# Optimization experiments

Hardware: AMD Instinct MI355X
Metric: run time of the kernel (lower is better)

## Reference

```python
import math
import jax, jax.numpy as jnp
import numpy as np


def bernstein_basis(s, k):
    # s: [N] in [0,1]; returns [N, k] with B_i(s) = C(k-1,i) s^i (1-s)^(k-1-i)
    l = k - 1
    i = jnp.arange(k, dtype=s.dtype)
    comb = jnp.asarray([math.comb(l, ii) for ii in range(k)], dtype=s.dtype)
    return comb * s[:, None] ** i * (1.0 - s[:, None]) ** (l - i)


def setup_inputs() -> dict:
    key = jax.random.key(0)
    k1, k2 = jax.random.split(key)
    N, kx, ky, kz = 1000000, 6, 6, 6
    vertices = jax.random.uniform(k1, (N, 3), dtype=jnp.float32) * 2.0 - 1.0  # in [-1,1]
    p = jax.random.uniform(k2, (3, kx, ky, kz), dtype=jnp.float32)
    return {"vertices": vertices, "p": p}


def reference(vertices, p):
    # vertices: [N,3] in [-1,1]; p: [3,kx,ky,kz]
    kx, ky, kz = p.shape[1], p.shape[2], p.shape[3]
    tar = (vertices + 1.0) * 0.5  # normalize_zero_to_one, [N,3]
    Bx = bernstein_basis(tar[:, 0], kx)  # [N,kx]
    By = bernstein_basis(tar[:, 1], ky)  # [N,ky]
    Bz = bernstein_basis(tar[:, 2], kz)  # [N,kz]
    # staged contraction replacing the kx*ky*kz loop of elementwise kernels
    t1 = jnp.einsum('nk,cijk->ncij', Bz, p)   # [N,3,kx,ky]
    t2 = jnp.einsum('nj,ncij->nci', By, t1)   # [N,3,kx]
    q = jnp.einsum('ni,nci->nc', Bx, t2)      # [N,3]
    q = 2.0 * q - 1.0  # normalize_minus_one_to_one
    return q[None, :, :]  # [1,N,3], matching q.permute(0,2,1)
```

## Files before the change

kernel.cpp:

```cpp
#include <hip/hip_runtime.h>

__device__ __constant__ float Mb[6][6] = {
    { 0.03125f, -0.15625f,  0.3125f, -0.3125f,  0.15625f, -0.03125f},
    { 0.15625f, -0.46875f,  0.3125f,  0.3125f, -0.46875f,  0.15625f},
    { 0.3125f,  -0.3125f,  -0.625f,   0.625f,   0.3125f,  -0.3125f },
    { 0.3125f,   0.3125f,  -0.625f,  -0.625f,   0.3125f,   0.3125f },
    { 0.15625f,  0.46875f,  0.3125f, -0.3125f, -0.46875f, -0.15625f},
    { 0.03125f,  0.15625f,  0.3125f,  0.3125f,  0.15625f,  0.03125f},
};

__global__ __launch_bounds__(256) void ffd_fused(const float* __restrict__ verts,
                                                 const float* __restrict__ p,
                                                 float* __restrict__ out, int N)
{
    __shared__ __align__(16) float b0[648];
    __shared__ __align__(16) float b1[648];
    const int t = threadIdx.x;

    for (int m = t; m < 648; m += 256) b0[m] = p[m];
    __syncthreads();

    for (int m = t; m < 648; m += 256) {
        const int dk = m % 6;
        const int base = (m / 6) * 6;
        float s = 0.f;
        #pragma unroll
        for (int k = 0; k < 6; ++k) s = fmaf(b0[base + k], Mb[k][dk], s);
        b1[m] = s;
    }
    __syncthreads();

    for (int m = t; m < 648; m += 256) {
        const int dk = m % 6;
        const int dj = (m / 6) % 6;
        const int ci = m / 36;
        float s = 0.f;
        #pragma unroll
        for (int j = 0; j < 6; ++j) s = fmaf(b1[(ci * 6 + j) * 6 + dk], Mb[j][dj], s);
        b0[m] = s;
    }
    __syncthreads();

    for (int m = t; m < 648; m += 256) {
        const int dk = m % 6;
        const int dj = (m / 6) % 6;
        const int di = (m / 36) % 6;
        const int c  = m / 216;
        float s = 0.f;
        #pragma unroll
        for (int i = 0; i < 6; ++i) s = fmaf(b0[((c * 6 + i) * 6 + dj) * 6 + dk], Mb[i][di], s);
        s *= 2.0f;
        if (di == 0 && dj == 0 && dk == 0) s -= 1.0f;
        b1[m] = s;
    }
    __syncthreads();

    const long long v0 = ((long long)blockIdx.x * 256 + t) * 4;
    if (v0 >= N) return;

    float x[4], y[4], z[4];
    const bool full = (v0 + 4 <= N);
    if (full) {
        const float4* vp = (const float4*)(verts + v0 * 3);
        const float4 f0 = vp[0], f1 = vp[1], f2 = vp[2];
        x[0] = f0.x; y[0] = f0.y; z[0] = f0.z;
        x[1] = f0.w; y[1] = f1.x; z[1] = f1.y;
        x[2] = f1.z; y[2] = f1.w; z[2] = f2.x;
        x[3] = f2.y; y[3] = f2.z; z[3] = f2.w;
    } else {
        for (int v = 0; v < 4; ++v) {
            long long n = v0 + v; if (n >= N) n = N - 1;
            x[v] = verts[n * 3 + 0]; y[v] = verts[n * 3 + 1]; z[v] = verts[n * 3 + 2];
        }
    }

    float res[12];
    #pragma unroll 1
    for (int c = 0; c < 3; ++c) {
        float q[4];
        #pragma unroll 1
        for (int ii = 0; ii < 6; ++ii) {
            const int i = 5 - ii;
            const float4* blk = (const float4*)(b1 + (c * 6 + i) * 36);
            float a[36];
            #pragma unroll
            for (int r = 0; r < 9; ++r) {
                const float4 f = blk[r];
                a[r * 4 + 0] = f.x; a[r * 4 + 1] = f.y;
                a[r * 4 + 2] = f.z; a[r * 4 + 3] = f.w;
            }
            float tj[4];
            #pragma unroll
            for (int jj = 0; jj < 6; ++jj) {
                const int j = 5 - jj;
                const float* Ak = a + j * 6;
                #pragma unroll
                for (int v = 0; v < 4; ++v) {
                    float s = fmaf(Ak[5], z[v], Ak[4]);
                    s = fmaf(s, z[v], Ak[3]);
                    s = fmaf(s, z[v], Ak[2]);
                    s = fmaf(s, z[v], Ak[1]);
                    s = fmaf(s, z[v], Ak[0]);
                    tj[v] = (jj == 0) ? s : fmaf(tj[v], y[v], s);
                }
            }
            #pragma unroll
            for (int v = 0; v < 4; ++v)
                q[v] = (ii == 0) ? tj[v] : fmaf(q[v], x[v], tj[v]);
        }
        #pragma unroll
        for (int v = 0; v < 4; ++v) res[v * 3 + c] = q[v];
    }

    if (full) {
        float4* op = (float4*)(out + v0 * 3);
        op[0] = make_float4(res[0], res[1], res[2],  res[3]);
        op[1] = make_float4(res[4], res[5], res[6],  res[7]);
        op[2] = make_float4(res[8], res[9], res[10], res[11]);
    } else {
        for (int v = 0; v < 4; ++v) {
            const long long n = v0 + v;
            if (n < N) {
                out[n * 3 + 0] = res[v * 3 + 0];
                out[n * 3 + 1] = res[v * 3 + 1];
                out[n * 3 + 2] = res[v * 3 + 2];
            }
        }
    }
}

extern "C" void kernel_launch(void* const* d_in, const int* in_sizes, int n_in,
                              void* d_out, int out_size, void* d_ws, size_t ws_size,
                              hipStream_t stream)
{
    const float* verts = (const float*)d_in[0];
    const float* p     = (const float*)d_in[1];
    float* out = (float*)d_out;
    const int N = in_sizes[0] / 3;

    const int nthreads = (N + 3) / 4;
    const int blocks = (nthreads + 255) / 256;
    ffd_fused<<<blocks, 256, 0, stream>>>(verts, p, out, N);
}
```

Baseline: 78.87 us.

## Split coefficient precompute into separate kernel and read coefficients via scalar loads

Moves the per-block Bernstein-to-monomial coefficient transform into a single-block kernel that writes 648 coefficients to workspace. The eval kernel then reads them with wave-uniform offsets (readfirstlane) so they can be fetched as scalar loads instead of from LDS. It also drops from 4 to 2 vertices per thread and unrolls the channel loop. This removes redundant per-block transform work and syncs, at the cost of an extra launch and half the per-thread work.

```diff
diff --git a/kernel.cpp b/kernel.cpp
--- a/kernel.cpp
+++ b/kernel.cpp
@@ -9,12 +9,11 @@
     { 0.03125f,  0.15625f,  0.3125f,  0.3125f,  0.15625f,  0.03125f},
 };
 
-__global__ __launch_bounds__(256) void ffd_fused(const float* __restrict__ verts,
-                                                 const float* __restrict__ p,
-                                                 float* __restrict__ out, int N)
+__global__ __launch_bounds__(256) void ffd_coeffs(const float* __restrict__ p,
+                                                  float* __restrict__ A)
 {
-    __shared__ __align__(16) float b0[648];
-    __shared__ __align__(16) float b1[648];
+    __shared__ float b0[648];
+    __shared__ float b1[648];
     const int t = threadIdx.x;
 
     for (int m = t; m < 648; m += 256) b0[m] = p[m];
@@ -51,74 +50,76 @@
         for (int i = 0; i < 6; ++i) s = fmaf(b0[((c * 6 + i) * 6 + dj) * 6 + dk], Mb[i][di], s);
         s *= 2.0f;
         if (di == 0 && dj == 0 && dk == 0) s -= 1.0f;
-        b1[m] = s;
+        A[m] = s;
     }
-    __syncthreads();
+}
 
-    const long long v0 = ((long long)blockIdx.x * 256 + t) * 4;
+__global__ __launch_bounds__(256) void ffd_eval(const float* __restrict__ verts,
+                                                const float* __restrict__ A,
+                                                float* __restrict__ out, int N)
+{
+    const long long v0 = ((long long)blockIdx.x * 256 + threadIdx.x) * 2;
     if (v0 >= N) return;
 
-    float x[4], y[4], z[4];
-    const bool full = (v0 + 4 <= N);
+    float x[2], y[2], z[2];
+    const bool full = (v0 + 2 <= N);
     if (full) {
-        const float4* vp = (const float4*)(verts + v0 * 3);
-        const float4 f0 = vp[0], f1 = vp[1], f2 = vp[2];
-        x[0] = f0.x; y[0] = f0.y; z[0] = f0.z;
-        x[1] = f0.w; y[1] = f1.x; z[1] = f1.y;
-        x[2] = f1.z; y[2] = f1.w; z[2] = f2.x;
-        x[3] = f2.y; y[3] = f2.z; z[3] = f2.w;
+        const float2* vp = (const float2*)(verts + v0 * 3);
+        const float2 f0 = vp[0], f1 = vp[1], f2 = vp[2];
+        x[0] = f0.x; y[0] = f0.y; z[0] = f1.x;
+        x[1] = f1.y; y[1] = f2.x; z[1] = f2.y;
     } else {
-        for (int v = 0; v < 4; ++v) {
+        for (int v = 0; v < 2; ++v) {
             long long n = v0 + v; if (n >= N) n = N - 1;
             x[v] = verts[n * 3 + 0]; y[v] = verts[n * 3 + 1]; z[v] = verts[n * 3 + 2];
         }
     }
 
-    float res[12];
-    #pragma unroll 1
+    float res[6];
+    #pragma unroll
     for (int c = 0; c < 3; ++c) {
-        float q[4];
+        float q0 = 0.f, q1 = 0.f;
         #pragma unroll 1
         for (int ii = 0; ii < 6; ++ii) {
             const int i = 5 - ii;
-            const float4* blk = (const float4*)(b1 + (c * 6 + i) * 36);
+            const int off = __builtin_amdgcn_readfirstlane((c * 6 + i) * 36);
+            const float* __restrict__ Ab = A + off;
             float a[36];
             #pragma unroll
-            for (int r = 0; r < 9; ++r) {
-                const float4 f = blk[r];
-                a[r * 4 + 0] = f.x; a[r * 4 + 1] = f.y;
-                a[r * 4 + 2] = f.z; a[r * 4 + 3] = f.w;
-            }
-            float tj[4];
+            for (int r = 0; r < 36; ++r) a[r] = Ab[r];
+
+            float t0 = 0.f, t1 = 0.f;
             #pragma unroll
             for (int jj = 0; jj < 6; ++jj) {
                 const int j = 5 - jj;
                 const float* Ak = a + j * 6;
-                #pragma unroll
-                for (int v = 0; v < 4; ++v) {
-                    float s = fmaf(Ak[5], z[v], Ak[4]);
-                    s = fmaf(s, z[v], Ak[3]);
-                    s = fmaf(s, z[v], Ak[2]);
-                    s = fmaf(s, z[v], Ak[1]);
-                    s = fmaf(s, z[v], Ak[0]);
-                    tj[v] = (jj == 0) ? s : fmaf(tj[v], y[v], s);
-                }
+                float s0 = fmaf(Ak[5], z[0], Ak[4]);
+                s0 = fmaf(s0, z[0], Ak[3]);
+                s0 = fmaf(s0, z[0], Ak[2]);
+                s0 = fmaf(s0, z[0], Ak[1]);
+                s0 = fmaf(s0, z[0], Ak[0]);
+                float s1 = fmaf(Ak[5], z[1], Ak[4]);
+                s1 = fmaf(s1, z[1], Ak[3]);
+                s1 = fmaf(s1, z[1], Ak[2]);
+                s1 = fmaf(s1, z[1], Ak[1]);
+                s1 = fmaf(s1, z[1], Ak[0]);
+                t0 = (jj == 0) ? s0 : fmaf(t0, y[0], s0);
+                t1 = (jj == 0) ? s1 : fmaf(t1, y[1], s1);
             }
-            #pragma unroll
-            for (int v = 0; v < 4; ++v)
-                q[v] = (ii == 0) ? tj[v] : fmaf(q[v], x[v], tj[v]);
+            q0 = (ii == 0) ? t0 : fmaf(q0, x[0], t0);
+            q1 = (ii == 0) ? t1 : fmaf(q1, x[1], t1);
         }
-        #pragma unroll
-        for (int v = 0; v < 4; ++v) res[v * 3 + c] = q[v];
+        res[c]     = q0;
+        res[3 + c] = q1;
     }
 
     if (full) {
-        float4* op = (float4*)(out + v0 * 3);
-        op[0] = make_float4(res[0], res[1], res[2],  res[3]);
-        op[1] = make_float4(res[4], res[5], res[6],  res[7]);
-        op[2] = make_float4(res[8], res[9], res[10], res[11]);
+        float2* op = (float2*)(out + v0 * 3);
+        op[0] = make_float2(res[0], res[1]);
+        op[1] = make_float2(res[2], res[3]);
+        op[2] = make_float2(res[4], res[5]);
     } else {
-        for (int v = 0; v < 4; ++v) {
+        for (int v = 0; v < 2; ++v) {
             const long long n = v0 + v;
             if (n < N) {
                 out[n * 3 + 0] = res[v * 3 + 0];
@@ -136,9 +137,12 @@
     const float* verts = (const float*)d_in[0];
     const float* p     = (const float*)d_in[1];
     float* out = (float*)d_out;
+    float* A   = (float*)d_ws;
     const int N = in_sizes[0] / 3;
 
-    const int nthreads = (N + 3) / 4;
+    ffd_coeffs<<<1, 256, 0, stream>>>(p, A);
+
+    const int nthreads = (N + 1) / 2;
     const int blocks = (nthreads + 255) / 256;
-    ffd_fused<<<blocks, 256, 0, stream>>>(verts, p, out, N);
+    ffd_eval<<<blocks, 256, 0, stream>>>(verts, A, out, N);
 }
```

Result: slower. 80.71 us (+2.3%).

## Split coefficient precompute into separate kernel and load coefficients via scalar loads

Applied to the files above, without the earlier changes.

Moves the Bernstein-to-monomial coefficient transform out of every block into a single-block precompute kernel that writes to workspace. The evaluation kernel then reads the 36-coefficient slices with inline-asm scalar loads into SGPRs instead of LDS reads, and fully unrolls the channel and i loops. This removes the redundant per-block shared-memory setup and barriers and the LDS traffic, at the cost of a second launch, a hard wait on each scalar load batch, and higher scalar register pressure.

```diff
diff --git a/kernel.cpp b/kernel.cpp
--- a/kernel.cpp
+++ b/kernel.cpp
@@ -9,12 +9,11 @@
     { 0.03125f,  0.15625f,  0.3125f,  0.3125f,  0.15625f,  0.03125f},
 };
 
-__global__ __launch_bounds__(256) void ffd_fused(const float* __restrict__ verts,
-                                                 const float* __restrict__ p,
-                                                 float* __restrict__ out, int N)
+__global__ __launch_bounds__(256) void ffd_coeffs(const float* __restrict__ p,
+                                                  float* __restrict__ A)
 {
-    __shared__ __align__(16) float b0[648];
-    __shared__ __align__(16) float b1[648];
+    __shared__ float b0[648];
+    __shared__ float b1[648];
     const int t = threadIdx.x;
 
     for (int m = t; m < 648; m += 256) b0[m] = p[m];
@@ -51,10 +50,18 @@
         for (int i = 0; i < 6; ++i) s = fmaf(b0[((c * 6 + i) * 6 + dj) * 6 + dk], Mb[i][di], s);
         s *= 2.0f;
         if (di == 0 && dj == 0 && dk == 0) s -= 1.0f;
-        b1[m] = s;
+        A[m] = s;
     }
-    __syncthreads();
+}
 
+typedef float f16v __attribute__((ext_vector_type(16)));
+typedef float f4v  __attribute__((ext_vector_type(4)));
+
+__global__ __launch_bounds__(256) void ffd_eval(const float* __restrict__ verts,
+                                                const float* __restrict__ A,
+                                                float* __restrict__ out, int N)
+{
+    const int t = threadIdx.x;
     const long long v0 = ((long long)blockIdx.x * 256 + t) * 4;
     if (v0 >= N) return;
 
@@ -75,20 +82,29 @@
     }
 
     float res[12];
-    #pragma unroll 1
+    #pragma unroll
     for (int c = 0; c < 3; ++c) {
         float q[4];
-        #pragma unroll 1
+        #pragma unroll
         for (int ii = 0; ii < 6; ++ii) {
             const int i = 5 - ii;
-            const float4* blk = (const float4*)(b1 + (c * 6 + i) * 36);
+            const float* Ab = A + (c * 6 + i) * 36;
+            f16v a0, a1; f4v a2;
+            asm volatile(
+                "s_load_dwordx16 %0, %3, 0x0\n\t"
+                "s_load_dwordx16 %1, %3, 0x40\n\t"
+                "s_load_dwordx4  %2, %3, 0x80\n\t"
+                "s_waitcnt lgkmcnt(0)"
+                : "=s"(a0), "=s"(a1), "=s"(a2)
+                : "s"(Ab));
             float a[36];
             #pragma unroll
-            for (int r = 0; r < 9; ++r) {
-                const float4 f = blk[r];
-                a[r * 4 + 0] = f.x; a[r * 4 + 1] = f.y;
-                a[r * 4 + 2] = f.z; a[r * 4 + 3] = f.w;
-            }
+            for (int r = 0; r < 16; ++r) a[r] = a0[r];
+            #pragma unroll
+            for (int r = 0; r < 16; ++r) a[16 + r] = a1[r];
+            #pragma unroll
+            for (int r = 0; r < 4; ++r) a[32 + r] = a2[r];
+
             float tj[4];
             #pragma unroll
             for (int jj = 0; jj < 6; ++jj) {
@@ -136,9 +152,12 @@
     const float* verts = (const float*)d_in[0];
     const float* p     = (const float*)d_in[1];
     float* out = (float*)d_out;
+    float* A   = (float*)d_ws;
     const int N = in_sizes[0] / 3;
+
+    ffd_coeffs<<<1, 256, 0, stream>>>(p, A);
 
     const int nthreads = (N + 3) / 4;
     const int blocks = (nthreads + 255) / 256;
-    ffd_fused<<<blocks, 256, 0, stream>>>(verts, p, out, N);
+    ffd_eval<<<blocks, 256, 0, stream>>>(verts, A, out, N);
 }
```

Result: slower. 104.2 us (+32.1%).

## Process eight vertices per thread with double-buffered LDS coefficient loads

Applied to the files above, without the earlier changes.

Each thread now handles eight vertices instead of four, so every coefficient block read from shared memory is reused across twice as many vertices. The i-loop is also split into ping-pong register buffers, so the next 36-float block is loaded while the current one is being evaluated, and the c loop is fully unrolled. The aim is to cut LDS traffic per vertex and hide LDS latency. In exchange, register pressure rises sharply (two 36-float buffers plus 8-wide state), which can lower occupancy, and the block count halves, so the per-block setup of the transformed coefficients is spread over more vertices.

```diff
diff --git a/kernel.cpp b/kernel.cpp
--- a/kernel.cpp
+++ b/kernel.cpp
@@ -55,70 +55,118 @@
     }
     __syncthreads();
 
-    const long long v0 = ((long long)blockIdx.x * 256 + t) * 4;
+    const long long v0 = ((long long)blockIdx.x * 256 + t) * 8;
     if (v0 >= N) return;
 
-    float x[4], y[4], z[4];
-    const bool full = (v0 + 4 <= N);
+    float x[8], y[8], z[8];
+    const bool full = (v0 + 8 <= N);
     if (full) {
         const float4* vp = (const float4*)(verts + v0 * 3);
-        const float4 f0 = vp[0], f1 = vp[1], f2 = vp[2];
+        float4 f0 = vp[0], f1 = vp[1], f2 = vp[2], f3 = vp[3], f4 = vp[4], f5 = vp[5];
         x[0] = f0.x; y[0] = f0.y; z[0] = f0.z;
         x[1] = f0.w; y[1] = f1.x; z[1] = f1.y;
         x[2] = f1.z; y[2] = f1.w; z[2] = f2.x;
         x[3] = f2.y; y[3] = f2.z; z[3] = f2.w;
+        x[4] = f3.x; y[4] = f3.y; z[4] = f3.z;
+        x[5] = f3.w; y[5] = f4.x; z[5] = f4.y;
+        x[6] = f4.z; y[6] = f4.w; z[6] = f5.x;
+        x[7] = f5.y; y[7] = f5.z; z[7] = f5.w;
     } else {
-        for (int v = 0; v < 4; ++v) {
+        for (int v = 0; v < 8; ++v) {
             long long n = v0 + v; if (n >= N) n = N - 1;
             x[v] = verts[n * 3 + 0]; y[v] = verts[n * 3 + 1]; z[v] = verts[n * 3 + 2];
         }
     }
 
-    float res[12];
-    #pragma unroll 1
+    float res[24];
+    #pragma unroll
     for (int c = 0; c < 3; ++c) {
-        float q[4];
-        #pragma unroll 1
-        for (int ii = 0; ii < 6; ++ii) {
-            const int i = 5 - ii;
-            const float4* blk = (const float4*)(b1 + (c * 6 + i) * 36);
-            float a[36];
+        float q[8];
+        #pragma unroll
+        for (int v = 0; v < 8; ++v) q[v] = 0.f;
+
+        float aA[36], aB[36];
+        {
+            const float4* blk = (const float4*)(b1 + c * 216 + 5 * 36);
             #pragma unroll
             for (int r = 0; r < 9; ++r) {
                 const float4 f = blk[r];
-                a[r * 4 + 0] = f.x; a[r * 4 + 1] = f.y;
-                a[r * 4 + 2] = f.z; a[r * 4 + 3] = f.w;
+                aA[r * 4 + 0] = f.x; aA[r * 4 + 1] = f.y;
+                aA[r * 4 + 2] = f.z; aA[r * 4 + 3] = f.w;
             }
-            float tj[4];
-            #pragma unroll
-            for (int jj = 0; jj < 6; ++jj) {
-                const int j = 5 - jj;
-                const float* Ak = a + j * 6;
+        }
+        #pragma unroll 1
+        for (int m = 0; m < 3; ++m) {
+            const int i0 = 5 - 2 * m;
+            {
+                const float4* blk = (const float4*)(b1 + c * 216 + (i0 - 1) * 36);
                 #pragma unroll
-                for (int v = 0; v < 4; ++v) {
-                    float s = fmaf(Ak[5], z[v], Ak[4]);
-                    s = fmaf(s, z[v], Ak[3]);
-                    s = fmaf(s, z[v], Ak[2]);
-                    s = fmaf(s, z[v], Ak[1]);
-                    s = fmaf(s, z[v], Ak[0]);
-                    tj[v] = (jj == 0) ? s : fmaf(tj[v], y[v], s);
+                for (int r = 0; r < 9; ++r) {
+                    const float4 f = blk[r];
+                    aB[r * 4 + 0] = f.x; aB[r * 4 + 1] = f.y;
+                    aB[r * 4 + 2] = f.z; aB[r * 4 + 3] = f.w;
                 }
             }
-            #pragma unroll
-            for (int v = 0; v < 4; ++v)
-                q[v] = (ii == 0) ? tj[v] : fmaf(q[v], x[v], tj[v]);
+            {
+                float tj[8];
+                #pragma unroll
+                for (int jj = 0; jj < 6; ++jj) {
+                    const int j = 5 - jj;
+                    const float* Ak = aA + j * 6;
+                    #pragma unroll
+                    for (int v = 0; v < 8; ++v) {
+                        float s = fmaf(Ak[5], z[v], Ak[4]);
+                        s = fmaf(s, z[v], Ak[3]);
+                        s = fmaf(s, z[v], Ak[2]);
+                        s = fmaf(s, z[v], Ak[1]);
+                        s = fmaf(s, z[v], Ak[0]);
+                        tj[v] = (jj == 0) ? s : fmaf(tj[v], y[v], s);
+                    }
+                }
+                #pragma unroll
+                for (int v = 0; v < 8; ++v) q[v] = fmaf(q[v], x[v], tj[v]);
+            }
+            if (m < 2) {
+                const float4* blk = (const float4*)(b1 + c * 216 + (i0 - 2) * 36);
+                #pragma unroll
+                for (int r = 0; r < 9; ++r) {
+                    const float4 f = blk[r];
+                    aA[r * 4 + 0] = f.x; aA[r * 4 + 1] = f.y;
+                    aA[r * 4 + 2] = f.z; aA[r * 4 + 3] = f.w;
+                }
+            }
+            {
+                float tj[8];
+                #pragma unroll
+                for (int jj = 0; jj < 6; ++jj) {
+                    const int j = 5 - jj;
+                    const float* Ak = aB + j * 6;
+                    #pragma unroll
+                    for (int v = 0; v < 8; ++v) {
+                        float s = fmaf(Ak[5], z[v], Ak[4]);
+                        s = fmaf(s, z[v], Ak[3]);
+                        s = fmaf(s, z[v], Ak[2]);
+                        s = fmaf(s, z[v], Ak[1]);
+                        s = fmaf(s, z[v], Ak[0]);
+                        tj[v] = (jj == 0) ? s : fmaf(tj[v], y[v], s);
+                    }
+                }
+                #pragma unroll
+                for (int v = 0; v < 8; ++v) q[v] = fmaf(q[v], x[v], tj[v]);
+            }
         }
         #pragma unroll
-        for (int v = 0; v < 4; ++v) res[v * 3 + c] = q[v];
+        for (int v = 0; v < 8; ++v) res[v * 3 + c] = q[v];
     }
 
     if (full) {
         float4* op = (float4*)(out + v0 * 3);
-        op[0] = make_float4(res[0], res[1], res[2],  res[3]);
-        op[1] = make_float4(res[4], res[5], res[6],  res[7]);
-        op[2] = make_float4(res[8], res[9], res[10], res[11]);
+        #pragma unroll
+        for (int r = 0; r < 6; ++r)
+            op[r] = make_float4(res[r * 4 + 0], res[r * 4 + 1],
+                                res[r * 4 + 2], res[r * 4 + 3]);
     } else {
-        for (int v = 0; v < 4; ++v) {
+        for (int v = 0; v < 8; ++v) {
             const long long n = v0 + v;
             if (n < N) {
                 out[n * 3 + 0] = res[v * 3 + 0];
@@ -138,7 +186,7 @@
     float* out = (float*)d_out;
     const int N = in_sizes[0] / 3;
 
-    const int nthreads = (N + 3) / 4;
+    const int nthreads = (N + 7) / 8;
     const int blocks = (nthreads + 255) / 256;
     ffd_fused<<<blocks, 256, 0, stream>>>(verts, p, out, N);
 }
```

Result: no change. 79.77 us (+1.1%).
